# Kernel optimization log

Measured on AMD Instinct MI355X. Metric: run time of the kernel, lower is better.

The kernel has to match this reference:

```python
import jax, jax.numpy as jnp
import numpy as np

N = 10000      # nodes
E = 320000     # directed edges (self-loops added in reference)
F_IN = 78      # atom features
D = 128        # embed_dim per head
H = 4          # heads in layer 1
G = 64         # graphs in batch
NEG_SLOPE = 0.2


def setup_inputs() -> dict:
    key = jax.random.key(0)
    ks = jax.random.split(key, 12)
    s = 0.05
    return {
        "x": jax.random.normal(ks[0], (N, F_IN), dtype=jnp.float32),
        "edge_index": jax.random.randint(ks[1], (2, E), 0, N, dtype=jnp.int64),
        "batch": jnp.sort(jax.random.randint(ks[2], (N,), 0, G, dtype=jnp.int64)),
        "Wl1": jax.random.normal(ks[3], (F_IN, H * D), dtype=jnp.float32) * s,
        "bl1": jnp.zeros((H * D,), jnp.float32),
        "Wr1": jax.random.normal(ks[4], (F_IN, H * D), dtype=jnp.float32) * s,
        "br1": jnp.zeros((H * D,), jnp.float32),
        "att1": jax.random.normal(ks[5], (H, D), dtype=jnp.float32) * s,
        "bias1": jnp.zeros((H * D,), jnp.float32),
        "Wl2": jax.random.normal(ks[6], (H * D, D), dtype=jnp.float32) * s,
        "bl2": jnp.zeros((D,), jnp.float32),
        "Wr2": jax.random.normal(ks[7], (H * D, D), dtype=jnp.float32) * s,
        "br2": jnp.zeros((D,), jnp.float32),
        "att2": jax.random.normal(ks[8], (1, D), dtype=jnp.float32) * s,
        "bias2": jnp.zeros((D,), jnp.float32),
    }


def gatv2_conv(x, src, dst, Wl, bl, Wr, br, att, bias, heads, out_ch):
    # x: [N, Fin]; src/dst: [Etot] (self-loops already included)
    n = x.shape[0]
    x_l = (x @ Wl + bl).reshape(n, heads, out_ch)  # source transform
    x_r = (x @ Wr + br).reshape(n, heads, out_ch)  # target transform
    # per-edge GATv2 score: att . LeakyReLU(x_l[src] + x_r[dst])
    e = x_l[src] + x_r[dst]                                   # [E, H, C]
    e = jnp.where(e > 0, e, NEG_SLOPE * e)                    # leaky_relu 0.2
    logits = jnp.einsum('ehc,hc->eh', e, att)                 # [E, H]
    # segment softmax over destination nodes (every node has a self-loop)
    seg_max = jax.ops.segment_max(logits, dst, num_segments=n)
    alpha = jnp.exp(logits - seg_max[dst])
    seg_sum = jax.ops.segment_sum(alpha, dst, num_segments=n)
    alpha = alpha / seg_sum[dst]                              # [E, H]
    # weighted scatter-sum aggregation of source features
    msg = alpha[:, :, None] * x_l[src]                        # [E, H, C]
    out = jax.ops.segment_sum(msg, dst, num_segments=n)       # [N, H, C]
    return out.reshape(n, heads * out_ch) + bias


def reference(x, edge_index, batch, Wl1, bl1, Wr1, br1, att1, bias1,
              Wl2, bl2, Wr2, br2, att2, bias2):
    n = x.shape[0]
    loops = jnp.arange(n, dtype=edge_index.dtype)
    src = jnp.concatenate([edge_index[0], loops])
    dst = jnp.concatenate([edge_index[1], loops])

    h = gatv2_conv(x, src, dst, Wl1, bl1, Wr1, br1, att1, bias1, H, D)
    h = jax.nn.elu(h)  # dropout: identity in eval mode
    h = gatv2_conv(h, src, dst, Wl2, bl2, Wr2, br2, att2, bias2, 1, D)
    h = jax.nn.elu(h)

    # global mean pool over graphs
    sums = jax.ops.segment_sum(h, batch, num_segments=G)          # [G, D]
    cnts = jax.ops.segment_sum(jnp.ones((n,), h.dtype), batch, num_segments=G)
    return sums / jnp.maximum(cnts, 1.0)[:, None]
```

## Files before the change

### kernel.cpp

```cpp
#include <hip/hip_runtime.h>
#include <hip/hip_fp16.h>
#include <math.h>

#define FIN 78
#define HD1 512
#define D2  128

__device__ __forceinline__ float lrelu(float x) { return x > 0.f ? x : 0.2f * x; }
__device__ __forceinline__ float elu(float x)   { return x > 0.f ? x : expf(x) - 1.f; }

__global__ void gemm1_k(const float* __restrict__ x,
                        const float* __restrict__ Wl, const float* __restrict__ bl,
                        const float* __restrict__ Wr, const float* __restrict__ br,
                        __half* __restrict__ xl, float* __restrict__ xr, int N)
{
    __shared__ float xs[8][FIN];
    int row0 = blockIdx.x * 8;
    int t = threadIdx.x;
    for (int idx = t; idx < 8 * FIN; idx += 256) {
        int r = idx / FIN, k = idx - r * FIN;
        int row = row0 + r;
        xs[r][k] = (row < N) ? x[(size_t)row * FIN + k] : 0.f;
    }
    __syncthreads();
    for (int i = 0; i < 4; ++i) {
        int j = t + i * 256;
        const float* W; int col; float b; bool isL;
        if (j < HD1) { W = Wl; col = j;       b = bl[col]; isL = true; }
        else         { W = Wr; col = j - HD1; b = br[col]; isL = false; }
        float acc[8];
#pragma unroll
        for (int r = 0; r < 8; ++r) acc[r] = b;
        for (int k = 0; k < FIN; ++k) {
            float w = W[k * HD1 + col];
#pragma unroll
            for (int r = 0; r < 8; ++r) acc[r] += xs[r][k] * w;
        }
#pragma unroll
        for (int r = 0; r < 8; ++r) {
            int row = row0 + r;
            if (row < N) {
                if (isL) xl[(size_t)row * HD1 + col] = __float2half(acc[r]);
                else     xr[(size_t)row * HD1 + col] = acc[r];
            }
        }
    }
}

__global__ void gemm2_k(const float* __restrict__ h,
                        const float* __restrict__ Wl, const float* __restrict__ bl,
                        const float* __restrict__ Wr, const float* __restrict__ br,
                        __half* __restrict__ xl, float* __restrict__ xr, int N)
{
    __shared__ float hs[8][HD1];
    int row0 = blockIdx.x * 8;
    int t = threadIdx.x;
    for (int idx = t; idx < 8 * HD1; idx += 256) {
        int r = idx >> 9, k = idx & 511;
        int row = row0 + r;
        hs[r][k] = (row < N) ? h[(size_t)row * HD1 + k] : 0.f;
    }
    __syncthreads();
    const float* W; int col; float b; bool isL;
    if (t < D2) { W = Wl; col = t;      b = bl[col]; isL = true; }
    else        { W = Wr; col = t - D2; b = br[col]; isL = false; }
    float acc[8];
#pragma unroll
    for (int r = 0; r < 8; ++r) acc[r] = b;
    for (int k = 0; k < HD1; ++k) {
        float w = W[k * D2 + col];
#pragma unroll
        for (int r = 0; r < 8; ++r) acc[r] += hs[r][k] * w;
    }
#pragma unroll
    for (int r = 0; r < 8; ++r) {
        int row = row0 + r;
        if (row < N) {
            if (isL) xl[(size_t)row * D2 + col] = __float2half(acc[r]);
            else     xr[(size_t)row * D2 + col] = acc[r];
        }
    }
}

__global__ void count_k(const int* __restrict__ ei, int E, int Etot, int* __restrict__ counts)
{
    int e = blockIdx.x * 256 + threadIdx.x;
    if (e >= Etot) return;
    int dst = (e < E) ? ei[E + e] : (e - E);
    atomicAdd(&counts[dst], 1);
}

__global__ void scan_k(const int* __restrict__ counts, int* __restrict__ row_ptr,
                       int* __restrict__ offs, int N)
{
    __shared__ int sdata[1024];
    int t = threadIdx.x;
    int chunk = (N + 1023) / 1024;
    int lo = t * chunk, hi = min(lo + chunk, N);
    int p = 0;
    for (int i = lo; i < hi; ++i) p += counts[i];
    sdata[t] = p;
    __syncthreads();
    for (int off = 1; off < 1024; off <<= 1) {
        int v = (t >= off) ? sdata[t - off] : 0;
        __syncthreads();
        sdata[t] += v;
        __syncthreads();
    }
    int run = sdata[t] - p;
    for (int i = lo; i < hi; ++i) { row_ptr[i] = run; offs[i] = run; run += counts[i]; }
    if (t == 1023) row_ptr[N] = sdata[1023];
}

__global__ void scatter_k(const int* __restrict__ ei, int E, int Etot,
                          int* __restrict__ offs, int* __restrict__ csr_src)
{
    int e = blockIdx.x * 256 + threadIdx.x;
    if (e >= Etot) return;
    int src, dst;
    if (e < E) { src = ei[e]; dst = ei[E + e]; } else { src = dst = e - E; }
    int pos = atomicAdd(&offs[dst], 1);
    csr_src[pos] = src;
}

__global__ __launch_bounds__(256, 8)
void fused1_k(const int* __restrict__ row_ptr, const int* __restrict__ csr_src,
              const __half* __restrict__ xl, const float* __restrict__ xr,
              const float* __restrict__ att, const float* __restrict__ bias,
              float* __restrict__ out)
{
    int v = blockIdx.x;
    int t = threadIdx.x;
    int w = t >> 6, lane = t & 63;
    int g = lane >> 4, sub = lane & 15;
    int base = row_ptr[v], deg = row_ptr[v + 1] - base;
    int c0 = (w << 7) + (sub << 3);

    float bb[8], at[8];
    {
        float4 b0 = *(const float4*)(xr + (size_t)v * HD1 + c0);
        float4 b1 = *(const float4*)(xr + (size_t)v * HD1 + c0 + 4);
        float4 t0 = *(const float4*)(att + c0);
        float4 t1 = *(const float4*)(att + c0 + 4);
        bb[0]=b0.x; bb[1]=b0.y; bb[2]=b0.z; bb[3]=b0.w;
        bb[4]=b1.x; bb[5]=b1.y; bb[6]=b1.z; bb[7]=b1.w;
        at[0]=t0.x; at[1]=t0.y; at[2]=t0.z; at[3]=t0.w;
        at[4]=t1.x; at[5]=t1.y; at[6]=t1.z; at[7]=t1.w;
    }

    float s = 0.f, a[8];
#pragma unroll
    for (int j = 0; j < 8; ++j) a[j] = 0.f;

    for (int i = g; i < deg; i += 4) {
        int src = csr_src[base + i];
        uint4 raw = *(const uint4*)(xl + (size_t)src * HD1 + c0);
        const __half2* hp = (const __half2*)&raw;
        float af[8];
#pragma unroll
        for (int j = 0; j < 4; ++j) {
            float2 f = __half22float2(hp[j]);
            af[2*j] = f.x; af[2*j+1] = f.y;
        }
        float p = 0.f;
#pragma unroll
        for (int j = 0; j < 8; ++j) p += at[j] * lrelu(af[j] + bb[j]);
#pragma unroll
        for (int off = 1; off < 16; off <<= 1) p += __shfl_xor(p, off);
        float e = __expf(p);
        s += e;
#pragma unroll
        for (int j = 0; j < 8; ++j) a[j] += e * af[j];
    }
    s += __shfl_xor(s, 16); s += __shfl_xor(s, 32);
#pragma unroll
    for (int j = 0; j < 8; ++j) { a[j] += __shfl_xor(a[j], 16); a[j] += __shfl_xor(a[j], 32); }

    if (g == 0) {
        float rs = 1.f / s;
        float o[8];
#pragma unroll
        for (int j = 0; j < 8; ++j) o[j] = elu(a[j] * rs + bias[c0 + j]);
        size_t ob = (size_t)v * HD1 + c0;
        *(float4*)(out + ob)     = make_float4(o[0], o[1], o[2], o[3]);
        *(float4*)(out + ob + 4) = make_float4(o[4], o[5], o[6], o[7]);
    }
}

__global__ __launch_bounds__(256, 8)
void fused2_k(const int* __restrict__ row_ptr, const int* __restrict__ csr_src,
              const __half* __restrict__ xl, const float* __restrict__ xr,
              const float* __restrict__ att, const float* __restrict__ bias,
              float* __restrict__ out, int N)
{
    int t = threadIdx.x;
    int w = t >> 6, lane = t & 63;
    int v = blockIdx.x * 4 + w;
    if (v >= N) return;
    int g = lane >> 4, sub = lane & 15;
    int base = row_ptr[v], deg = row_ptr[v + 1] - base;
    int c0 = sub << 3;

    float bb[8], at[8];
    {
        float4 b0 = *(const float4*)(xr + (size_t)v * D2 + c0);
        float4 b1 = *(const float4*)(xr + (size_t)v * D2 + c0 + 4);
        float4 t0 = *(const float4*)(att + c0);
        float4 t1 = *(const float4*)(att + c0 + 4);
        bb[0]=b0.x; bb[1]=b0.y; bb[2]=b0.z; bb[3]=b0.w;
        bb[4]=b1.x; bb[5]=b1.y; bb[6]=b1.z; bb[7]=b1.w;
        at[0]=t0.x; at[1]=t0.y; at[2]=t0.z; at[3]=t0.w;
        at[4]=t1.x; at[5]=t1.y; at[6]=t1.z; at[7]=t1.w;
    }

    float s = 0.f, a[8];
#pragma unroll
    for (int j = 0; j < 8; ++j) a[j] = 0.f;

    for (int i = g; i < deg; i += 4) {
        int src = csr_src[base + i];
        uint4 raw = *(const uint4*)(xl + (size_t)src * D2 + c0);
        const __half2* hp = (const __half2*)&raw;
        float af[8];
#pragma unroll
        for (int j = 0; j < 4; ++j) {
            float2 f = __half22float2(hp[j]);
            af[2*j] = f.x; af[2*j+1] = f.y;
        }
        float p = 0.f;
#pragma unroll
        for (int j = 0; j < 8; ++j) p += at[j] * lrelu(af[j] + bb[j]);
#pragma unroll
        for (int off = 1; off < 16; off <<= 1) p += __shfl_xor(p, off);
        float e = __expf(p);
        s += e;
#pragma unroll
        for (int j = 0; j < 8; ++j) a[j] += e * af[j];
    }
    s += __shfl_xor(s, 16); s += __shfl_xor(s, 32);
#pragma unroll
    for (int j = 0; j < 8; ++j) { a[j] += __shfl_xor(a[j], 16); a[j] += __shfl_xor(a[j], 32); }

    if (g == 0) {
        float rs = 1.f / s;
        float o[8];
#pragma unroll
        for (int j = 0; j < 8; ++j) o[j] = elu(a[j] * rs + bias[c0 + j]);
        size_t ob = (size_t)v * D2 + c0;
        *(float4*)(out + ob)     = make_float4(o[0], o[1], o[2], o[3]);
        *(float4*)(out + ob + 4) = make_float4(o[4], o[5], o[6], o[7]);
    }
}

__global__ void gb_k(const int* __restrict__ batch, int* __restrict__ gb, int N, int G)
{
    int g = blockIdx.x * 128 + threadIdx.x;
    if (g > G) return;
    int lo = 0, hi = N;
    while (lo < hi) {
        int mid = (lo + hi) >> 1;
        if (batch[mid] < g) lo = mid + 1; else hi = mid;
    }
    gb[g] = lo;
}

__global__ void pool2_k(const int* __restrict__ gb, const float* __restrict__ h,
                        float* __restrict__ out)
{
    __shared__ float part[D2];
    int g = blockIdx.x;
    int t = threadIdx.x;
    int c = t & 127, half = t >> 7;
    int lo = gb[g], hi = gb[g + 1];
    float acc = 0.f;
    for (int v = lo + half; v < hi; v += 2)
        acc += h[(size_t)v * D2 + c];
    if (half == 1) part[c] = acc;
    __syncthreads();
    if (half == 0) {
        float tot = acc + part[c];
        float cnt = (float)max(hi - lo, 1);
        out[(size_t)g * D2 + c] = tot / cnt;
    }
}

extern "C" void kernel_launch(void* const* d_in, const int* in_sizes, int n_in,
                              void* d_out, int out_size, void* d_ws, size_t ws_size,
                              hipStream_t stream)
{
    const float* x    = (const float*)d_in[0];
    const int*   ei   = (const int*)d_in[1];
    const int*   batch= (const int*)d_in[2];
    const float* Wl1  = (const float*)d_in[3];
    const float* bl1  = (const float*)d_in[4];
    const float* Wr1  = (const float*)d_in[5];
    const float* br1  = (const float*)d_in[6];
    const float* att1 = (const float*)d_in[7];
    const float* bias1= (const float*)d_in[8];
    const float* Wl2  = (const float*)d_in[9];
    const float* bl2  = (const float*)d_in[10];
    const float* Wr2  = (const float*)d_in[11];
    const float* br2  = (const float*)d_in[12];
    const float* att2 = (const float*)d_in[13];
    const float* bias2= (const float*)d_in[14];
    float* out = (float*)d_out;

    int N    = in_sizes[2];
    int E    = in_sizes[1] / 2;
    int Etot = E + N;
    int G    = out_size / D2;

    char* ws = (char*)d_ws;
    size_t off = 0;
    auto alloc = [&](size_t bytes) -> void* {
        void* p = ws + off;
        off = (off + bytes + 255) & ~(size_t)255;
        return p;
    };
    __half* xl1h   = (__half*)alloc((size_t)N * HD1 * 2);
    float*  xr1    = (float*)alloc((size_t)N * HD1 * 4);
    float*  h1     = (float*)alloc((size_t)N * HD1 * 4);
    __half* xl2h   = (__half*)alloc((size_t)N * D2 * 2);
    float*  xr2    = (float*)alloc((size_t)N * D2 * 4);
    float*  h2     = (float*)alloc((size_t)N * D2 * 4);
    int*    counts = (int*)alloc((size_t)(N + 1) * 4);
    int*    offs   = (int*)alloc((size_t)(N + 1) * 4);
    int*    row_ptr= (int*)alloc((size_t)(N + 1) * 4);
    int*    csr_src= (int*)alloc((size_t)Etot * 4);
    int*    gb     = (int*)alloc((size_t)(G + 1) * 4);

    hipMemsetAsync(counts, 0, (size_t)(N + 1) * 4, stream);
    gemm1_k<<<(N + 7) / 8, 256, 0, stream>>>(x, Wl1, bl1, Wr1, br1, xl1h, xr1, N);
    count_k<<<(Etot + 255) / 256, 256, 0, stream>>>(ei, E, Etot, counts);
    scan_k<<<1, 1024, 0, stream>>>(counts, row_ptr, offs, N);
    scatter_k<<<(Etot + 255) / 256, 256, 0, stream>>>(ei, E, Etot, offs, csr_src);
    fused1_k<<<N, 256, 0, stream>>>(row_ptr, csr_src, xl1h, xr1, att1, bias1, h1);
    gemm2_k<<<(N + 7) / 8, 256, 0, stream>>>(h1, Wl2, bl2, Wr2, br2, xl2h, xr2, N);
    fused2_k<<<(N + 3) / 4, 256, 0, stream>>>(row_ptr, csr_src, xl2h, xr2, att2, bias2, h2, N);
    gb_k<<<1, 128, 0, stream>>>(batch, gb, N, G);
    pool2_k<<<G, 256, 0, stream>>>(gb, h2, out);
}
```

Measured before the change: 284.8 us.

## Store layer-1 output in fp16 and use packed fdot2 in second GEMM

The first attention-aggregation kernel now writes its ELU output as fp16, which halves that intermediate's write and read traffic. The second GEMM reads fp16 activations, loads them into shared memory with 128-bit loads, and uses packed fp16 dot-product instructions against a transposed fp16 copy of the weights. That copy is built each call by a small new conversion kernel. Each thread now computes two output columns for 8 rows of a 16-row tile, which should lower GEMM compute and memory cost, at the price of fp16 rounding on activations and weights.

```diff
diff --git a/kernel.cpp b/kernel.cpp
--- a/kernel.cpp
+++ b/kernel.cpp
@@ -5,6 +5,10 @@
 #define FIN 78
 #define HD1 512
 #define D2  128
+
+typedef _Float16 f16x2 __attribute__((ext_vector_type(2)));
+union U2H { unsigned u; f16x2 h; __half2 hh; };
+__device__ __forceinline__ f16x2 u2h(unsigned u) { U2H x; x.u = u; return x.h; }
 
 __device__ __forceinline__ float lrelu(float x) { return x > 0.f ? x : 0.2f * x; }
 __device__ __forceinline__ float elu(float x)   { return x > 0.f ? x : expf(x) - 1.f; }
@@ -47,37 +51,73 @@
     }
 }
 
-__global__ void gemm2_k(const float* __restrict__ h,
-                        const float* __restrict__ Wl, const float* __restrict__ bl,
-                        const float* __restrict__ Wr, const float* __restrict__ br,
-                        __half* __restrict__ xl, float* __restrict__ xr, int N)
-{
-    __shared__ float hs[8][HD1];
-    int row0 = blockIdx.x * 8;
-    int t = threadIdx.x;
-    for (int idx = t; idx < 8 * HD1; idx += 256) {
-        int r = idx >> 9, k = idx & 511;
+__global__ void cvtW2_k(const float* __restrict__ Wl, const float* __restrict__ Wr,
+                        unsigned* __restrict__ Wt)
+{
+    int idx = blockIdx.x * 256 + threadIdx.x;
+    int col = idx >> 8, k2 = idx & 255;
+    float w0, w1;
+    if (col < D2) { w0 = Wl[(2 * k2) * D2 + col];       w1 = Wl[(2 * k2 + 1) * D2 + col]; }
+    else          { int cc = col - D2;
+                    w0 = Wr[(2 * k2) * D2 + cc];        w1 = Wr[(2 * k2 + 1) * D2 + cc]; }
+    U2H x; x.hh = __floats2half2_rn(w0, w1);
+    Wt[idx] = x.u;
+}
+
+__global__ __launch_bounds__(256, 4)
+void gemm2_k(const __half* __restrict__ h, const unsigned* __restrict__ Wt,
+             const float* __restrict__ bl, const float* __restrict__ br,
+             __half* __restrict__ xl, float* __restrict__ xr, int N)
+{
+    __shared__ unsigned hs[16][256];
+    int row0 = blockIdx.x * 16;
+    int t = threadIdx.x;
+    for (int idx = t; idx < 16 * 64; idx += 256) {
+        int r = idx >> 6, q = idx & 63;
         int row = row0 + r;
-        hs[r][k] = (row < N) ? h[(size_t)row * HD1 + k] : 0.f;
+        uint4 val = make_uint4(0u, 0u, 0u, 0u);
+        if (row < N) val = *(const uint4*)(h + (size_t)row * HD1 + q * 8);
+        *(uint4*)&hs[r][q * 4] = val;
     }
     __syncthreads();
-    const float* W; int col; float b; bool isL;
-    if (t < D2) { W = Wl; col = t;      b = bl[col]; isL = true; }
-    else        { W = Wr; col = t - D2; b = br[col]; isL = false; }
-    float acc[8];
-#pragma unroll
-    for (int r = 0; r < 8; ++r) acc[r] = b;
-    for (int k = 0; k < HD1; ++k) {
-        float w = W[k * D2 + col];
-#pragma unroll
-        for (int r = 0; r < 8; ++r) acc[r] += hs[r][k] * w;
-    }
-#pragma unroll
-    for (int r = 0; r < 8; ++r) {
-        int row = row0 + r;
-        if (row < N) {
-            if (isL) xl[(size_t)row * D2 + col] = __float2half(acc[r]);
-            else     xr[(size_t)row * D2 + col] = acc[r];
+
+    int c = t & 127, rg = t >> 7;
+    const unsigned* w0p = Wt + (size_t)(2 * c)     * 256;
+    const unsigned* w1p = Wt + (size_t)(2 * c + 1) * 256;
+    float acc[8][2];
+#pragma unroll
+    for (int r = 0; r < 8; ++r) { acc[r][0] = 0.f; acc[r][1] = 0.f; }
+
+    for (int k2 = 0; k2 < 256; ++k2) {
+        f16x2 w0 = u2h(w0p[k2]);
+        f16x2 w1 = u2h(w1p[k2]);
+#pragma unroll
+        for (int r = 0; r < 8; ++r) {
+            f16x2 hv = u2h(hs[rg * 8 + r][k2]);
+            acc[r][0] = __builtin_amdgcn_fdot2(hv, w0, acc[r][0], false);
+            acc[r][1] = __builtin_amdgcn_fdot2(hv, w1, acc[r][1], false);
+        }
+    }
+
+    if (c < 64) {
+        int cc = 2 * c;
+        float b0 = bl[cc], b1 = bl[cc + 1];
+#pragma unroll
+        for (int r = 0; r < 8; ++r) {
+            int row = row0 + rg * 8 + r;
+            if (row < N)
+                *(__half2*)(xl + (size_t)row * D2 + cc) =
+                    __floats2half2_rn(acc[r][0] + b0, acc[r][1] + b1);
+        }
+    } else {
+        int cc = 2 * c - 128;
+        float b0 = br[cc], b1 = br[cc + 1];
+#pragma unroll
+        for (int r = 0; r < 8; ++r) {
+            int row = row0 + rg * 8 + r;
+            if (row < N)
+                *(float2*)(xr + (size_t)row * D2 + cc) =
+                    make_float2(acc[r][0] + b0, acc[r][1] + b1);
         }
     }
 }
@@ -127,7 +167,7 @@
 void fused1_k(const int* __restrict__ row_ptr, const int* __restrict__ csr_src,
               const __half* __restrict__ xl, const float* __restrict__ xr,
               const float* __restrict__ att, const float* __restrict__ bias,
-              float* __restrict__ out)
+              __half* __restrict__ out)
 {
     int v = blockIdx.x;
     int t = threadIdx.x;
@@ -178,12 +218,12 @@
 
     if (g == 0) {
         float rs = 1.f / s;
-        float o[8];
-#pragma unroll
-        for (int j = 0; j < 8; ++j) o[j] = elu(a[j] * rs + bias[c0 + j]);
-        size_t ob = (size_t)v * HD1 + c0;
-        *(float4*)(out + ob)     = make_float4(o[0], o[1], o[2], o[3]);
-        *(float4*)(out + ob + 4) = make_float4(o[4], o[5], o[6], o[7]);
+        union { __half2 h2[4]; uint4 u; } pk;
+#pragma unroll
+        for (int j = 0; j < 4; ++j)
+            pk.h2[j] = __floats2half2_rn(elu(a[2*j]   * rs + bias[c0 + 2*j]),
+                                         elu(a[2*j+1] * rs + bias[c0 + 2*j+1]));
+        *(uint4*)(out + (size_t)v * HD1 + c0) = pk.u;
     }
 }
 
@@ -317,25 +357,27 @@
         off = (off + bytes + 255) & ~(size_t)255;
         return p;
     };
-    __half* xl1h   = (__half*)alloc((size_t)N * HD1 * 2);
-    float*  xr1    = (float*)alloc((size_t)N * HD1 * 4);
-    float*  h1     = (float*)alloc((size_t)N * HD1 * 4);
-    __half* xl2h   = (__half*)alloc((size_t)N * D2 * 2);
-    float*  xr2    = (float*)alloc((size_t)N * D2 * 4);
-    float*  h2     = (float*)alloc((size_t)N * D2 * 4);
-    int*    counts = (int*)alloc((size_t)(N + 1) * 4);
-    int*    offs   = (int*)alloc((size_t)(N + 1) * 4);
-    int*    row_ptr= (int*)alloc((size_t)(N + 1) * 4);
-    int*    csr_src= (int*)alloc((size_t)Etot * 4);
-    int*    gb     = (int*)alloc((size_t)(G + 1) * 4);
+    __half*   xl1h   = (__half*)alloc((size_t)N * HD1 * 2);
+    float*    xr1    = (float*)alloc((size_t)N * HD1 * 4);
+    __half*   h1h    = (__half*)alloc((size_t)N * HD1 * 2);
+    __half*   xl2h   = (__half*)alloc((size_t)N * D2 * 2);
+    float*    xr2    = (float*)alloc((size_t)N * D2 * 4);
+    float*    h2     = (float*)alloc((size_t)N * D2 * 4);
+    unsigned* Wt2    = (unsigned*)alloc((size_t)256 * 256 * 4);
+    int*      counts = (int*)alloc((size_t)(N + 1) * 4);
+    int*      offs   = (int*)alloc((size_t)(N + 1) * 4);
+    int*      row_ptr= (int*)alloc((size_t)(N + 1) * 4);
+    int*      csr_src= (int*)alloc((size_t)Etot * 4);
+    int*      gb     = (int*)alloc((size_t)(G + 1) * 4);
 
     hipMemsetAsync(counts, 0, (size_t)(N + 1) * 4, stream);
+    cvtW2_k<<<256, 256, 0, stream>>>(Wl2, Wr2, Wt2);
     gemm1_k<<<(N + 7) / 8, 256, 0, stream>>>(x, Wl1, bl1, Wr1, br1, xl1h, xr1, N);
     count_k<<<(Etot + 255) / 256, 256, 0, stream>>>(ei, E, Etot, counts);
     scan_k<<<1, 1024, 0, stream>>>(counts, row_ptr, offs, N);
     scatter_k<<<(Etot + 255) / 256, 256, 0, stream>>>(ei, E, Etot, offs, csr_src);
-    fused1_k<<<N, 256, 0, stream>>>(row_ptr, csr_src, xl1h, xr1, att1, bias1, h1);
-    gemm2_k<<<(N + 7) / 8, 256, 0, stream>>>(h1, Wl2, bl2, Wr2, br2, xl2h, xr2, N);
+    fused1_k<<<N, 256, 0, stream>>>(row_ptr, csr_src, xl1h, xr1, att1, bias1, h1h);
+    gemm2_k<<<(N + 15) / 16, 256, 0, stream>>>(h1h, Wt2, bl2, br2, xl2h, xr2, N);
     fused2_k<<<(N + 3) / 4, 256, 0, stream>>>(row_ptr, csr_src, xl2h, xr2, att2, bias2, h2, N);
     gb_k<<<1, 128, 0, stream>>>(batch, gb, N, G);
     pool2_k<<<G, 256, 0, stream>>>(gb, h2, out);
```

After: 276.5 us. -2.9%, faster.
